# Kernel tuning notes

Hardware: AMD Instinct MI355X
Metric: run time of the kernel (lower is better)

## Reference

```python
import jax, jax.numpy as jnp
import numpy as np

MARGIN = 1.0
B, D = 8192, 128
NUM_CLASSES = 100


def _pairwise_dist(x):
    # Euclidean cdist via ||a-b||^2 = ||a||^2 + ||b||^2 - 2 a.b  (same math as torch.cdist p=2)
    sq = jnp.sum(x * x, axis=-1)                       # [B]
    d2 = sq[:, None] + sq[None, :] - 2.0 * (x @ x.T)    # [B, B]
    d2 = jnp.maximum(d2, 0.0)
    safe = jnp.where(d2 > 0, d2, 1.0)                   # guard sqrt(0) grad
    return jnp.where(d2 > 0, jnp.sqrt(safe), 0.0)


def setup_inputs() -> dict:
    key = jax.random.key(0)
    k1, k2 = jax.random.split(key)
    embeddings = jax.random.normal(k1, (B, D), dtype=jnp.float32)
    labels = jax.random.randint(k2, (B,), 0, NUM_CLASSES, dtype=jnp.int64)
    return {"embeddings": embeddings, "labels": labels}


def reference(embeddings, labels):
    n = embeddings.shape[0]
    d = _pairwise_dist(embeddings)                      # [B, B]
    same = labels[:, None] == labels[None, :]           # [B, B]
    eye = jnp.eye(n, dtype=bool)
    pos_mask = same & ~eye                              # positives, diagonal removed
    neg_mask = ~same                                    # negatives
    # row-wise masked min of positives / max of negatives (inf/-inf when empty, as in original)
    pos_dists = jnp.min(jnp.where(pos_mask, d, jnp.inf), axis=1)   # [B]
    neg_dists = jnp.max(jnp.where(neg_mask, d, -jnp.inf), axis=1)  # [B]
    loss = jnp.mean(jnp.maximum(pos_dists - neg_dists + MARGIN, 0.0))
    return loss
```

## Files before the change

kernel.cpp:

```cpp
#include <hip/hip_runtime.h>
#include <hip/hip_bf16.h>
#include <math.h>

#define B 8192
#define D 128
#define NCHUNK 16
#define CPC (B / NCHUNK)
#define CT 64
#define NCT (CPC / CT)
#define BROWS 256
#define MARGIN 1.0f

typedef short short8 __attribute__((ext_vector_type(8)));
typedef float f32x4 __attribute__((ext_vector_type(4)));


__device__ inline ushort f2bf(float f) {
    __hip_bfloat16 h = __float2bfloat16(f);
    ushort u; __builtin_memcpy(&u, &h, 2); return u;
}
__device__ inline float bf2f(ushort u) {
    unsigned int i = ((unsigned)u) << 16; float f; __builtin_memcpy(&f, &i, 4); return f;
}

__device__ inline void gload_lds16(const void* gsrc, void* ldst) {
    __builtin_amdgcn_global_load_lds(
        (const __attribute__((address_space(1))) unsigned int*)gsrc,
        (__attribute__((address_space(3))) unsigned int*)ldst,
        16, 0, 0);
}

__global__ void mmcl_sqn_kernel(const float* __restrict__ X,
                                float* __restrict__ sqn,
                                float* __restrict__ out) {
    const int wave = threadIdx.x >> 6;
    const int lane = threadIdx.x & 63;
    const int row  = blockIdx.x * 4 + wave;
    const float2 v = *(const float2*)(X + (size_t)row * D + lane * 2);
    float s = v.x * v.x + v.y * v.y;
    #pragma unroll
    for (int off = 32; off; off >>= 1) s += __shfl_down(s, off);
    if (lane == 0) sqn[row] = s;
    if (blockIdx.x == 0 && threadIdx.x == 0) *out = 0.0f;
}

__global__ void mmcl_prep_kernel(const float* __restrict__ X,
                                 ushort* __restrict__ Xh) {
    const int t  = blockIdx.x * 256 + threadIdx.x;
    const int r  = t >> 4;
    const int kg = t & 15;
    const float4 v0 = *(const float4*)(X + (size_t)r * D + kg * 8);
    const float4 v1 = *(const float4*)(X + (size_t)r * D + kg * 8 + 4);
    const float xs[8] = {v0.x, v0.y, v0.z, v0.w, v1.x, v1.y, v1.z, v1.w};
    short8 hv, lv;
    #pragma unroll
    for (int i = 0; i < 8; ++i) {
        const float x = xs[i];
        const ushort h = f2bf(x);
        hv[i] = (short)h;
        lv[i] = (short)f2bf(x - bf2f(h));
    }
    const int s = r & 7;
    ushort* rp = Xh + (size_t)r * 256;
    *(short8*)(rp + ((kg ^ s) << 3))        = hv;
    *(short8*)(rp + (((16 + kg) ^ s) << 3)) = lv;
}

__global__ __launch_bounds__(256, 2) void mmcl_mfma_kernel(
    const ushort* __restrict__ Xh, const float* __restrict__ sqn,
    const int* __restrict__ lab,
    float* __restrict__ ppos, float* __restrict__ pneg)
{
    __shared__ ushort lds[2][CT * 256];
    const int tid  = threadIdx.x;
    const int wid  = tid >> 6;
    const int lane = tid & 63;
    const int lhi  = lane >> 4;
    const int llo  = lane & 15;
    const int R    = blockIdx.x * BROWS + wid * 64;
    const int C0   = blockIdx.y * CPC;

    short8 a_hi[4][4], a_lo[4][4];
    #pragma unroll
    for (int m = 0; m < 4; ++m) {
        const int row = R + m * 16 + llo;
        const int s = row & 7;
        const ushort* rp = Xh + (size_t)row * 256;
        #pragma unroll
        for (int kf = 0; kf < 4; ++kf) {
            const int g = kf * 4 + lhi;
            a_hi[m][kf] = *(const short8*)(rp + ((g ^ s) << 3));
            a_lo[m][kf] = *(const short8*)(rp + (((16 + g) ^ s) << 3));
        }
    }

    int labR[4][4];
    #pragma unroll
    for (int m = 0; m < 4; ++m)
        #pragma unroll
        for (int r = 0; r < 4; ++r)
            labR[m][r] = lab[R + m * 16 + lhi * 4 + r];

    float minpos[4][4], maxneg[4][4];
    #pragma unroll
    for (int m = 0; m < 4; ++m)
        #pragma unroll
        for (int r = 0; r < 4; ++r) { minpos[m][r] = INFINITY; maxneg[m][r] = -INFINITY; }

    auto stage = [&](int buf, int t) {
        const char* g = (const char*)(Xh + (size_t)(C0 + t * CT) * 256) + wid * 8192 + lane * 16;
        char* l = (char*)&lds[buf][0] + wid * 8192;
        #pragma unroll
        for (int i = 0; i < 8; ++i)
            gload_lds16(g + i * 1024, l + i * 1024);
    };

    stage(0, 0);

    for (int t = 0; t < NCT; ++t) {
        const int cur = t & 1;
        __syncthreads();
        if (t + 1 < NCT) stage(cur ^ 1, t + 1);

        const int colbase = C0 + t * CT;
        #pragma unroll
        for (int n = 0; n < 4; ++n) {
            const int cl = n * 16 + llo;
            const int s = cl & 7;
            const ushort* bp = &lds[cur][cl * 256];
            f32x4 acc[4];
            #pragma unroll
            for (int m = 0; m < 4; ++m) acc[m] = (f32x4){0.f, 0.f, 0.f, 0.f};

            #pragma unroll
            for (int kf = 0; kf < 4; ++kf) {
                const int g = kf * 4 + lhi;
                const short8 b_hi = *(const short8*)(bp + ((g ^ s) << 3));
                const short8 b_lo = *(const short8*)(bp + (((16 + g) ^ s) << 3));
                #pragma unroll
                for (int m = 0; m < 4; ++m) {
                    acc[m] = __builtin_amdgcn_mfma_f32_16x16x32_bf16(a_hi[m][kf], b_hi, acc[m], 0, 0, 0);
                    acc[m] = __builtin_amdgcn_mfma_f32_16x16x32_bf16(a_hi[m][kf], b_lo, acc[m], 0, 0, 0);
                    acc[m] = __builtin_amdgcn_mfma_f32_16x16x32_bf16(a_lo[m][kf], b_hi, acc[m], 0, 0, 0);
                }
            }

            const int col  = colbase + cl;
            const float sqc = sqn[col];
            const int   lc  = lab[col];
            #pragma unroll
            for (int m = 0; m < 4; ++m) {
                const int rowb = R + m * 16 + lhi * 4;
                #pragma unroll
                for (int r = 0; r < 4; ++r) {
                    const float v = fmaf(-2.0f, acc[m][r], sqc);
                    const bool same = (labR[m][r] == lc);
                    const bool diag = (rowb + r == col);
                    if (same && !diag) minpos[m][r] = fminf(minpos[m][r], v);
                    if (!same)         maxneg[m][r] = fmaxf(maxneg[m][r], v);
                }
            }
        }
    }

    #pragma unroll
    for (int m = 0; m < 4; ++m)
        #pragma unroll
        for (int r = 0; r < 4; ++r) {
            float mp = minpos[m][r], mn = maxneg[m][r];
            #pragma unroll
            for (int off = 1; off < 16; off <<= 1) {
                mp = fminf(mp, __shfl_xor(mp, off));
                mn = fmaxf(mn, __shfl_xor(mn, off));
            }
            if (llo == 0) {
                const int row = R + m * 16 + lhi * 4 + r;
                ppos[(size_t)blockIdx.y * B + row] = mp;
                pneg[(size_t)blockIdx.y * B + row] = mn;
            }
        }
}

__global__ void mmcl_final_kernel(const float* __restrict__ sqn,
                                  const float* __restrict__ ppos,
                                  const float* __restrict__ pneg,
                                  float* __restrict__ out)
{
    const int row = blockIdx.x * 256 + threadIdx.x;
    float mp = INFINITY, mn = -INFINITY;
    #pragma unroll
    for (int c = 0; c < NCHUNK; ++c) {
        mp = fminf(mp, ppos[(size_t)c * B + row]);
        mn = fmaxf(mn, pneg[(size_t)c * B + row]);
    }
    const float sq  = sqn[row];
    const float pos = isinf(mp) ? INFINITY : sqrtf(fmaxf(sq + mp, 0.f));
    const float neg = (mn == -INFINITY) ? -INFINITY : sqrtf(fmaxf(sq + mn, 0.f));
    const float term = fmaxf(pos - neg + MARGIN, 0.f);

    float s = term;
    #pragma unroll
    for (int off = 32; off; off >>= 1) s += __shfl_down(s, off);
    __shared__ float wsum[4];
    const int wave = threadIdx.x >> 6, lane = threadIdx.x & 63;
    if (lane == 0) wsum[wave] = s;
    __syncthreads();
    if (threadIdx.x == 0)
        atomicAdd(out, (wsum[0] + wsum[1] + wsum[2] + wsum[3]) * (1.0f / B));
}

extern "C" void kernel_launch(void* const* d_in, const int* in_sizes, int n_in,
                              void* d_out, int out_size, void* d_ws, size_t ws_size,
                              hipStream_t stream) {
    (void)in_sizes; (void)n_in; (void)out_size; (void)ws_size;
    const float* X   = (const float*)d_in[0];
    const int*   lab = (const int*)d_in[1];
    float* out = (float*)d_out;

    float*  sqn  = (float*)d_ws;
    float*  ppos = sqn + B;
    float*  pneg = ppos + (size_t)NCHUNK * B;
    ushort* Xh   = (ushort*)(pneg + (size_t)NCHUNK * B);

    mmcl_sqn_kernel<<<B / 4, 256, 0, stream>>>(X, sqn, out);
    mmcl_prep_kernel<<<(B * 16) / 256, 256, 0, stream>>>(X, Xh);
    mmcl_mfma_kernel<<<dim3(B / BROWS, NCHUNK), 256, 0, stream>>>(Xh, sqn, lab, ppos, pneg);
    mmcl_final_kernel<<<B / 256, 256, 0, stream>>>(sqn, ppos, pneg, out);
}
```

Baseline: 111.8 us.

## Fuse norm into prep, atomic min/max partials, prefetch column data, split diagonal path

Folds the squared-norm computation and output/partial initialisation into the prep kernel, which removes one launch. Per-chunk partial arrays are replaced by order-preserving encoded atomicMin/atomicMax into per-row buffers, so the final kernel reads two values per row instead of sixteen. Inside the MFMA loop it prefetches column norms and labels one tile ahead, raises wave priority around the MFMA block, and uses a cheaper epilogue without the diagonal check for tiles that cannot contain the diagonal. The cost is atomics contention and the extra complexity of encoding and decoding the floats.

```diff
diff --git a/kernel.cpp b/kernel.cpp
--- a/kernel.cpp
+++ b/kernel.cpp
@@ -22,6 +22,14 @@
 __device__ inline float bf2f(ushort u) {
     unsigned int i = ((unsigned)u) << 16; float f; __builtin_memcpy(&f, &i, 4); return f;
 }
+__device__ inline unsigned fenc(float f) {
+    unsigned u = __float_as_uint(f);
+    return (u & 0x80000000u) ? ~u : (u | 0x80000000u);
+}
+__device__ inline float fdec(unsigned m) {
+    unsigned u = (m & 0x80000000u) ? (m & 0x7FFFFFFFu) : ~m;
+    return __uint_as_float(u);
+}
 
 __device__ inline void gload_lds16(const void* gsrc, void* ldst) {
     __builtin_amdgcn_global_load_lds(
@@ -30,28 +38,26 @@
         16, 0, 0);
 }
 
-__global__ void mmcl_sqn_kernel(const float* __restrict__ X,
-                                float* __restrict__ sqn,
-                                float* __restrict__ out) {
-    const int wave = threadIdx.x >> 6;
-    const int lane = threadIdx.x & 63;
-    const int row  = blockIdx.x * 4 + wave;
-    const float2 v = *(const float2*)(X + (size_t)row * D + lane * 2);
-    float s = v.x * v.x + v.y * v.y;
-    #pragma unroll
-    for (int off = 32; off; off >>= 1) s += __shfl_down(s, off);
-    if (lane == 0) sqn[row] = s;
-    if (blockIdx.x == 0 && threadIdx.x == 0) *out = 0.0f;
-}
-
 __global__ void mmcl_prep_kernel(const float* __restrict__ X,
-                                 ushort* __restrict__ Xh) {
+                                 ushort* __restrict__ Xh,
+                                 float* __restrict__ sqn,
+                                 unsigned* __restrict__ posE,
+                                 unsigned* __restrict__ negE,
+                                 float* __restrict__ out) {
     const int t  = blockIdx.x * 256 + threadIdx.x;
     const int r  = t >> 4;
     const int kg = t & 15;
     const float4 v0 = *(const float4*)(X + (size_t)r * D + kg * 8);
     const float4 v1 = *(const float4*)(X + (size_t)r * D + kg * 8 + 4);
     const float xs[8] = {v0.x, v0.y, v0.z, v0.w, v1.x, v1.y, v1.z, v1.w};
+
+    float s = 0.f;
+    #pragma unroll
+    for (int i = 0; i < 8; ++i) s = fmaf(xs[i], xs[i], s);
+    #pragma unroll
+    for (int off = 1; off < 16; off <<= 1) s += __shfl_xor(s, off);
+    if (kg == 0) sqn[r] = s;
+
     short8 hv, lv;
     #pragma unroll
     for (int i = 0; i < 8; ++i) {
@@ -60,16 +66,19 @@
         hv[i] = (short)h;
         lv[i] = (short)f2bf(x - bf2f(h));
     }
-    const int s = r & 7;
+    const int sw = r & 7;
     ushort* rp = Xh + (size_t)r * 256;
-    *(short8*)(rp + ((kg ^ s) << 3))        = hv;
-    *(short8*)(rp + (((16 + kg) ^ s) << 3)) = lv;
+    *(short8*)(rp + ((kg ^ sw) << 3))        = hv;
+    *(short8*)(rp + (((16 + kg) ^ sw) << 3)) = lv;
+
+    if (t < B) { posE[t] = 0xFF800000u; negE[t] = 0x007FFFFFu; }
+    if (t == 0) *out = 0.0f;
 }
 
 __global__ __launch_bounds__(256, 2) void mmcl_mfma_kernel(
     const ushort* __restrict__ Xh, const float* __restrict__ sqn,
     const int* __restrict__ lab,
-    float* __restrict__ ppos, float* __restrict__ pneg)
+    unsigned* __restrict__ posE, unsigned* __restrict__ negE)
 {
     __shared__ ushort lds[2][CT * 256];
     const int tid  = threadIdx.x;
@@ -77,20 +86,21 @@
     const int lane = tid & 63;
     const int lhi  = lane >> 4;
     const int llo  = lane & 15;
-    const int R    = blockIdx.x * BROWS + wid * 64;
+    const int Rblk = blockIdx.x * BROWS;
+    const int R    = Rblk + wid * 64;
     const int C0   = blockIdx.y * CPC;
 
     short8 a_hi[4][4], a_lo[4][4];
     #pragma unroll
     for (int m = 0; m < 4; ++m) {
         const int row = R + m * 16 + llo;
-        const int s = row & 7;
+        const int sw = row & 7;
         const ushort* rp = Xh + (size_t)row * 256;
         #pragma unroll
         for (int kf = 0; kf < 4; ++kf) {
             const int g = kf * 4 + lhi;
-            a_hi[m][kf] = *(const short8*)(rp + ((g ^ s) << 3));
-            a_lo[m][kf] = *(const short8*)(rp + (((16 + g) ^ s) << 3));
+            a_hi[m][kf] = *(const short8*)(rp + ((g ^ sw) << 3));
+            a_lo[m][kf] = *(const short8*)(rp + (((16 + g) ^ sw) << 3));
         }
     }
 
@@ -117,26 +127,51 @@
 
     stage(0, 0);
 
+    float sqc_pf[4]; int lc_pf[4];
+    #pragma unroll
+    for (int n = 0; n < 4; ++n) {
+        const int col = C0 + n * 16 + llo;
+        sqc_pf[n] = sqn[col];
+        lc_pf[n]  = lab[col];
+    }
+
+    #pragma unroll 2
     for (int t = 0; t < NCT; ++t) {
         const int cur = t & 1;
         __syncthreads();
         if (t + 1 < NCT) stage(cur ^ 1, t + 1);
 
         const int colbase = C0 + t * CT;
+
+        float sqc_u[4]; int lc_u[4];
+        #pragma unroll
+        for (int n = 0; n < 4; ++n) { sqc_u[n] = sqc_pf[n]; lc_u[n] = lc_pf[n]; }
+        if (t + 1 < NCT) {
+            #pragma unroll
+            for (int n = 0; n < 4; ++n) {
+                const int col = colbase + CT + n * 16 + llo;
+                sqc_pf[n] = sqn[col];
+                lc_pf[n]  = lab[col];
+            }
+        }
+
+        const bool hasdiag = (colbase + CT > Rblk) && (colbase < Rblk + BROWS);
+
         #pragma unroll
         for (int n = 0; n < 4; ++n) {
             const int cl = n * 16 + llo;
-            const int s = cl & 7;
+            const int sw = cl & 7;
             const ushort* bp = &lds[cur][cl * 256];
             f32x4 acc[4];
             #pragma unroll
             for (int m = 0; m < 4; ++m) acc[m] = (f32x4){0.f, 0.f, 0.f, 0.f};
 
+            __builtin_amdgcn_s_setprio(1);
             #pragma unroll
             for (int kf = 0; kf < 4; ++kf) {
                 const int g = kf * 4 + lhi;
-                const short8 b_hi = *(const short8*)(bp + ((g ^ s) << 3));
-                const short8 b_lo = *(const short8*)(bp + (((16 + g) ^ s) << 3));
+                const short8 b_hi = *(const short8*)(bp + ((g ^ sw) << 3));
+                const short8 b_lo = *(const short8*)(bp + (((16 + g) ^ sw) << 3));
                 #pragma unroll
                 for (int m = 0; m < 4; ++m) {
                     acc[m] = __builtin_amdgcn_mfma_f32_16x16x32_bf16(a_hi[m][kf], b_hi, acc[m], 0, 0, 0);
@@ -144,20 +179,34 @@
                     acc[m] = __builtin_amdgcn_mfma_f32_16x16x32_bf16(a_lo[m][kf], b_hi, acc[m], 0, 0, 0);
                 }
             }
-
-            const int col  = colbase + cl;
-            const float sqc = sqn[col];
-            const int   lc  = lab[col];
-            #pragma unroll
-            for (int m = 0; m < 4; ++m) {
-                const int rowb = R + m * 16 + lhi * 4;
+            __builtin_amdgcn_s_setprio(0);
+
+            const int col   = colbase + cl;
+            const float sqc = sqc_u[n];
+            const int   lc  = lc_u[n];
+            if (hasdiag) {
                 #pragma unroll
-                for (int r = 0; r < 4; ++r) {
-                    const float v = fmaf(-2.0f, acc[m][r], sqc);
-                    const bool same = (labR[m][r] == lc);
-                    const bool diag = (rowb + r == col);
-                    if (same && !diag) minpos[m][r] = fminf(minpos[m][r], v);
-                    if (!same)         maxneg[m][r] = fmaxf(maxneg[m][r], v);
+                for (int m = 0; m < 4; ++m) {
+                    const int rowb = R + m * 16 + lhi * 4;
+                    #pragma unroll
+                    for (int r = 0; r < 4; ++r) {
+                        const float v = fmaf(-2.0f, acc[m][r], sqc);
+                        const bool same = (labR[m][r] == lc);
+                        const bool diag = (rowb + r == col);
+                        if (same && !diag) minpos[m][r] = fminf(minpos[m][r], v);
+                        if (!same)         maxneg[m][r] = fmaxf(maxneg[m][r], v);
+                    }
+                }
+            } else {
+                #pragma unroll
+                for (int m = 0; m < 4; ++m) {
+                    #pragma unroll
+                    for (int r = 0; r < 4; ++r) {
+                        const float v = fmaf(-2.0f, acc[m][r], sqc);
+                        const bool same = (labR[m][r] == lc);
+                        if (same) minpos[m][r] = fminf(minpos[m][r], v);
+                        else      maxneg[m][r] = fmaxf(maxneg[m][r], v);
+                    }
                 }
             }
         }
@@ -175,24 +224,20 @@
             }
             if (llo == 0) {
                 const int row = R + m * 16 + lhi * 4 + r;
-                ppos[(size_t)blockIdx.y * B + row] = mp;
-                pneg[(size_t)blockIdx.y * B + row] = mn;
+                atomicMin(&posE[row], fenc(mp));
+                atomicMax(&negE[row], fenc(mn));
             }
         }
 }
 
 __global__ void mmcl_final_kernel(const float* __restrict__ sqn,
-                                  const float* __restrict__ ppos,
-                                  const float* __restrict__ pneg,
+                                  const unsigned* __restrict__ posE,
+                                  const unsigned* __restrict__ negE,
                                   float* __restrict__ out)
 {
     const int row = blockIdx.x * 256 + threadIdx.x;
-    float mp = INFINITY, mn = -INFINITY;
-    #pragma unroll
-    for (int c = 0; c < NCHUNK; ++c) {
-        mp = fminf(mp, ppos[(size_t)c * B + row]);
-        mn = fmaxf(mn, pneg[(size_t)c * B + row]);
-    }
+    const float mp = fdec(posE[row]);
+    const float mn = fdec(negE[row]);
     const float sq  = sqn[row];
     const float pos = isinf(mp) ? INFINITY : sqrtf(fmaxf(sq + mp, 0.f));
     const float neg = (mn == -INFINITY) ? -INFINITY : sqrtf(fmaxf(sq + mn, 0.f));
@@ -217,13 +262,12 @@
     const int*   lab = (const int*)d_in[1];
     float* out = (float*)d_out;
 
-    float*  sqn  = (float*)d_ws;
-    float*  ppos = sqn + B;
-    float*  pneg = ppos + (size_t)NCHUNK * B;
-    ushort* Xh   = (ushort*)(pneg + (size_t)NCHUNK * B);
-
-    mmcl_sqn_kernel<<<B / 4, 256, 0, stream>>>(X, sqn, out);
-    mmcl_prep_kernel<<<(B * 16) / 256, 256, 0, stream>>>(X, Xh);
-    mmcl_mfma_kernel<<<dim3(B / BROWS, NCHUNK), 256, 0, stream>>>(Xh, sqn, lab, ppos, pneg);
-    mmcl_final_kernel<<<B / 256, 256, 0, stream>>>(sqn, ppos, pneg, out);
-}
+    float*    sqn  = (float*)d_ws;
+    unsigned* posE = (unsigned*)(sqn + B);
+    unsigned* negE = posE + B;
+    ushort*   Xh   = (ushort*)(negE + B);
+
+    mmcl_prep_kernel<<<(B * 16) / 256, 256, 0, stream>>>(X, Xh, sqn, posE, negE, out);
+    mmcl_mfma_kernel<<<dim3(B / BROWS, NCHUNK), 256, 0, stream>>>(Xh, sqn, lab, posE, negE);
+    mmcl_final_kernel<<<B / 256, 256, 0, stream>>>(sqn, posE, negE, out);
+}
```

Result: slower. 171.9 us (+53.7%).

## Drop LDS staging, read B fragments from global, fuse sqn into prep

Applied to the files above, without the earlier changes.

The MFMA kernel no longer stages column tiles through double-buffered LDS. Each wave now reads B fragments straight from global/L2, with a smaller 32-row tile per wave, 32 column chunks and a launch bound of 3 blocks per SM. The squared-norm kernel is folded into the prep kernel, and the swizzle is removed. Other additions are split accumulators for MFMA ILP, s_setprio around the MFMAs, prefetch of column sqn and labels, branchless min/max, and a diagonal check only on tiles that can contain the diagonal. This cuts a launch and LDS sync overhead in exchange for more global/L2 traffic and less A-fragment reuse per B load.

```diff
diff --git a/kernel.cpp b/kernel.cpp
--- a/kernel.cpp
+++ b/kernel.cpp
@@ -4,11 +4,10 @@
 
 #define B 8192
 #define D 128
-#define NCHUNK 16
+#define NCHUNK 32
 #define CPC (B / NCHUNK)
-#define CT 64
-#define NCT (CPC / CT)
-#define BROWS 256
+#define NCG (CPC / 16)
+#define RPB 128
 #define MARGIN 1.0f
 
 typedef short short8 __attribute__((ext_vector_type(8)));
@@ -23,35 +22,24 @@
     unsigned int i = ((unsigned)u) << 16; float f; __builtin_memcpy(&f, &i, 4); return f;
 }
 
-__device__ inline void gload_lds16(const void* gsrc, void* ldst) {
-    __builtin_amdgcn_global_load_lds(
-        (const __attribute__((address_space(1))) unsigned int*)gsrc,
-        (__attribute__((address_space(3))) unsigned int*)ldst,
-        16, 0, 0);
-}
-
-__global__ void mmcl_sqn_kernel(const float* __restrict__ X,
-                                float* __restrict__ sqn,
-                                float* __restrict__ out) {
-    const int wave = threadIdx.x >> 6;
-    const int lane = threadIdx.x & 63;
-    const int row  = blockIdx.x * 4 + wave;
-    const float2 v = *(const float2*)(X + (size_t)row * D + lane * 2);
-    float s = v.x * v.x + v.y * v.y;
-    #pragma unroll
-    for (int off = 32; off; off >>= 1) s += __shfl_down(s, off);
-    if (lane == 0) sqn[row] = s;
-    if (blockIdx.x == 0 && threadIdx.x == 0) *out = 0.0f;
-}
-
 __global__ void mmcl_prep_kernel(const float* __restrict__ X,
-                                 ushort* __restrict__ Xh) {
+                                 ushort* __restrict__ Xh,
+                                 float* __restrict__ sqn,
+                                 float* __restrict__ out) {
     const int t  = blockIdx.x * 256 + threadIdx.x;
     const int r  = t >> 4;
     const int kg = t & 15;
     const float4 v0 = *(const float4*)(X + (size_t)r * D + kg * 8);
     const float4 v1 = *(const float4*)(X + (size_t)r * D + kg * 8 + 4);
     const float xs[8] = {v0.x, v0.y, v0.z, v0.w, v1.x, v1.y, v1.z, v1.w};
+
+    float s = 0.f;
+    #pragma unroll
+    for (int i = 0; i < 8; ++i) s = fmaf(xs[i], xs[i], s);
+    #pragma unroll
+    for (int off = 1; off < 16; off <<= 1) s += __shfl_xor(s, off);
+    if (kg == 0) sqn[r] = s;
+
     short8 hv, lv;
     #pragma unroll
     for (int i = 0; i < 8; ++i) {
@@ -60,111 +48,125 @@
         hv[i] = (short)h;
         lv[i] = (short)f2bf(x - bf2f(h));
     }
-    const int s = r & 7;
     ushort* rp = Xh + (size_t)r * 256;
-    *(short8*)(rp + ((kg ^ s) << 3))        = hv;
-    *(short8*)(rp + (((16 + kg) ^ s) << 3)) = lv;
-}
-
-__global__ __launch_bounds__(256, 2) void mmcl_mfma_kernel(
+    *(short8*)(rp + (kg << 3))         = hv;
+    *(short8*)(rp + ((16 + kg) << 3))  = lv;
+
+    if (t == 0) *out = 0.0f;
+}
+
+__global__ __launch_bounds__(256, 3) void mmcl_mfma_kernel(
     const ushort* __restrict__ Xh, const float* __restrict__ sqn,
     const int* __restrict__ lab,
     float* __restrict__ ppos, float* __restrict__ pneg)
 {
-    __shared__ ushort lds[2][CT * 256];
     const int tid  = threadIdx.x;
-    const int wid  = tid >> 6;
+    const int w    = tid >> 6;
     const int lane = tid & 63;
     const int lhi  = lane >> 4;
     const int llo  = lane & 15;
-    const int R    = blockIdx.x * BROWS + wid * 64;
+    const int R    = blockIdx.x * RPB + w * 32;
     const int C0   = blockIdx.y * CPC;
-
-    short8 a_hi[4][4], a_lo[4][4];
-    #pragma unroll
-    for (int m = 0; m < 4; ++m) {
-        const int row = R + m * 16 + llo;
-        const int s = row & 7;
-        const ushort* rp = Xh + (size_t)row * 256;
+    const int chnk = blockIdx.y;
+
+    short8 a_hi[2][4], a_lo[2][4];
+    #pragma unroll
+    for (int m = 0; m < 2; ++m) {
+        const ushort* rp = Xh + (size_t)(R + m * 16 + llo) * 256;
         #pragma unroll
         for (int kf = 0; kf < 4; ++kf) {
             const int g = kf * 4 + lhi;
-            a_hi[m][kf] = *(const short8*)(rp + ((g ^ s) << 3));
-            a_lo[m][kf] = *(const short8*)(rp + (((16 + g) ^ s) << 3));
-        }
-    }
-
-    int labR[4][4];
-    #pragma unroll
-    for (int m = 0; m < 4; ++m)
+            a_hi[m][kf] = *(const short8*)(rp + (g << 3));
+            a_lo[m][kf] = *(const short8*)(rp + ((16 + g) << 3));
+        }
+    }
+
+    int labR[2][4];
+    #pragma unroll
+    for (int m = 0; m < 2; ++m)
         #pragma unroll
         for (int r = 0; r < 4; ++r)
             labR[m][r] = lab[R + m * 16 + lhi * 4 + r];
 
-    float minpos[4][4], maxneg[4][4];
-    #pragma unroll
-    for (int m = 0; m < 4; ++m)
+    float minpos[2][4], maxneg[2][4];
+    #pragma unroll
+    for (int m = 0; m < 2; ++m)
         #pragma unroll
         for (int r = 0; r < 4; ++r) { minpos[m][r] = INFINITY; maxneg[m][r] = -INFINITY; }
 
-    auto stage = [&](int buf, int t) {
-        const char* g = (const char*)(Xh + (size_t)(C0 + t * CT) * 256) + wid * 8192 + lane * 16;
-        char* l = (char*)&lds[buf][0] + wid * 8192;
-        #pragma unroll
-        for (int i = 0; i < 8; ++i)
-            gload_lds16(g + i * 1024, l + i * 1024);
-    };
-
-    stage(0, 0);
-
-    for (int t = 0; t < NCT; ++t) {
-        const int cur = t & 1;
-        __syncthreads();
-        if (t + 1 < NCT) stage(cur ^ 1, t + 1);
-
-        const int colbase = C0 + t * CT;
-        #pragma unroll
-        for (int n = 0; n < 4; ++n) {
-            const int cl = n * 16 + llo;
-            const int s = cl & 7;
-            const ushort* bp = &lds[cur][cl * 256];
-            f32x4 acc[4];
-            #pragma unroll
-            for (int m = 0; m < 4; ++m) acc[m] = (f32x4){0.f, 0.f, 0.f, 0.f};
-
-            #pragma unroll
-            for (int kf = 0; kf < 4; ++kf) {
-                const int g = kf * 4 + lhi;
-                const short8 b_hi = *(const short8*)(bp + ((g ^ s) << 3));
-                const short8 b_lo = *(const short8*)(bp + (((16 + g) ^ s) << 3));
-                #pragma unroll
-                for (int m = 0; m < 4; ++m) {
-                    acc[m] = __builtin_amdgcn_mfma_f32_16x16x32_bf16(a_hi[m][kf], b_hi, acc[m], 0, 0, 0);
-                    acc[m] = __builtin_amdgcn_mfma_f32_16x16x32_bf16(a_hi[m][kf], b_lo, acc[m], 0, 0, 0);
-                    acc[m] = __builtin_amdgcn_mfma_f32_16x16x32_bf16(a_lo[m][kf], b_hi, acc[m], 0, 0, 0);
-                }
-            }
-
-            const int col  = colbase + cl;
-            const float sqc = sqn[col];
-            const int   lc  = lab[col];
-            #pragma unroll
-            for (int m = 0; m < 4; ++m) {
+    float sq_pf = sqn[C0 + llo];
+    int   lc_pf = lab[C0 + llo];
+
+    for (int cg = 0; cg < NCG; ++cg) {
+        const int c = C0 + cg * 16;
+        const float sq_c = sq_pf;
+        const int   lc   = lc_pf;
+        if (cg + 1 < NCG) {
+            sq_pf = sqn[c + 16 + llo];
+            lc_pf = lab[c + 16 + llo];
+        }
+
+        const ushort* bp = Xh + (size_t)(c + llo) * 256;
+        f32x4 acc[2][2];
+        #pragma unroll
+        for (int m = 0; m < 2; ++m) {
+            acc[m][0] = (f32x4){0.f, 0.f, 0.f, 0.f};
+            acc[m][1] = (f32x4){0.f, 0.f, 0.f, 0.f};
+        }
+
+        __builtin_amdgcn_s_setprio(1);
+        #pragma unroll
+        for (int kf = 0; kf < 4; ++kf) {
+            const int g = kf * 4 + lhi;
+            const short8 b_hi = *(const short8*)(bp + (g << 3));
+            const short8 b_lo = *(const short8*)(bp + ((16 + g) << 3));
+            const int p = kf & 1;
+            #pragma unroll
+            for (int m = 0; m < 2; ++m) {
+                acc[m][p] = __builtin_amdgcn_mfma_f32_16x16x32_bf16(a_hi[m][kf], b_hi, acc[m][p], 0, 0, 0);
+                acc[m][p] = __builtin_amdgcn_mfma_f32_16x16x32_bf16(a_hi[m][kf], b_lo, acc[m][p], 0, 0, 0);
+                acc[m][p] = __builtin_amdgcn_mfma_f32_16x16x32_bf16(a_lo[m][kf], b_hi, acc[m][p], 0, 0, 0);
+            }
+        }
+        __builtin_amdgcn_s_setprio(0);
+
+        const int col = c + llo;
+        const bool hd = (c < R + 32) && (c + 16 > R);
+        if (hd) {
+            #pragma unroll
+            for (int m = 0; m < 2; ++m) {
                 const int rowb = R + m * 16 + lhi * 4;
                 #pragma unroll
                 for (int r = 0; r < 4; ++r) {
-                    const float v = fmaf(-2.0f, acc[m][r], sqc);
+                    float v = acc[m][0][r] + acc[m][1][r];
+                    v = fmaf(-2.0f, v, sq_c);
                     const bool same = (labR[m][r] == lc);
                     const bool diag = (rowb + r == col);
-                    if (same && !diag) minpos[m][r] = fminf(minpos[m][r], v);
-                    if (!same)         maxneg[m][r] = fmaxf(maxneg[m][r], v);
+                    const float vp = (same && !diag) ? v : INFINITY;
+                    const float vn = same ? -INFINITY : v;
+                    minpos[m][r] = fminf(minpos[m][r], vp);
+                    maxneg[m][r] = fmaxf(maxneg[m][r], vn);
                 }
             }
-        }
-    }
-
-    #pragma unroll
-    for (int m = 0; m < 4; ++m)
+        } else {
+            #pragma unroll
+            for (int m = 0; m < 2; ++m) {
+                #pragma unroll
+                for (int r = 0; r < 4; ++r) {
+                    float v = acc[m][0][r] + acc[m][1][r];
+                    v = fmaf(-2.0f, v, sq_c);
+                    const bool same = (labR[m][r] == lc);
+                    const float vp = same ? v : INFINITY;
+                    const float vn = same ? -INFINITY : v;
+                    minpos[m][r] = fminf(minpos[m][r], vp);
+                    maxneg[m][r] = fmaxf(maxneg[m][r], vn);
+                }
+            }
+        }
+    }
+
+    #pragma unroll
+    for (int m = 0; m < 2; ++m)
         #pragma unroll
         for (int r = 0; r < 4; ++r) {
             float mp = minpos[m][r], mn = maxneg[m][r];
@@ -175,8 +177,8 @@
             }
             if (llo == 0) {
                 const int row = R + m * 16 + lhi * 4 + r;
-                ppos[(size_t)blockIdx.y * B + row] = mp;
-                pneg[(size_t)blockIdx.y * B + row] = mn;
+                ppos[(size_t)chnk * B + row] = mp;
+                pneg[(size_t)chnk * B + row] = mn;
             }
         }
 }
@@ -222,8 +224,7 @@
     float*  pneg = ppos + (size_t)NCHUNK * B;
     ushort* Xh   = (ushort*)(pneg + (size_t)NCHUNK * B);
 
-    mmcl_sqn_kernel<<<B / 4, 256, 0, stream>>>(X, sqn, out);
-    mmcl_prep_kernel<<<(B * 16) / 256, 256, 0, stream>>>(X, Xh);
-    mmcl_mfma_kernel<<<dim3(B / BROWS, NCHUNK), 256, 0, stream>>>(Xh, sqn, lab, ppos, pneg);
+    mmcl_prep_kernel<<<(B * 16) / 256, 256, 0, stream>>>(X, Xh, sqn, out);
+    mmcl_mfma_kernel<<<dim3(B / RPB, NCHUNK), 256, 0, stream>>>(Xh, sqn, lab, ppos, pneg);
     mmcl_final_kernel<<<B / 256, 256, 0, stream>>>(sqn, ppos, pneg, out);
 }
```

Result: slower. 219.5 us (+96.2%).
